# Kernel optimization log

Measured on AMD Instinct MI355X. Metric: run time of the kernel, lower is better.

## Reference

```python
import jax, jax.numpy as jnp
import numpy as np

B = 65536      # batch
N_IN = 784     # n_input_neurons
D = 10         # n_neurons_per_hidd_bank
NB = 10        # banks per layer (layer0 = input banks 0-9, layer1 = output banks 10-19)
N_OUT = 10     # n_output_neurons
N_HIDD_BANKS = 20


def setup_inputs() -> dict:
    key = jax.random.key(0)
    ks = jax.random.split(key, 10)
    s_in = 1.0 / np.sqrt(N_IN)
    s_d = 1.0 / np.sqrt(D)
    return {
        "x": jax.random.normal(ks[0], (B, N_IN), dtype=jnp.float32),
        # input-bank linears: 784 -> 10, one per input bank
        "W_in": jax.random.uniform(ks[1], (NB, N_IN, D), jnp.float32, -s_in, s_in),
        "b_in": jax.random.uniform(ks[2], (NB, D), jnp.float32, -s_in, s_in),
        # gate linears per (source, target) connection: 10 -> 1
        "W_gate": jax.random.uniform(ks[3], (NB, NB, D), jnp.float32, -s_d, s_d),
        "b_gate": jax.random.uniform(ks[4], (NB, NB), jnp.float32, -s_d, s_d),
        # data linears per (source, target) connection: 10 -> 10
        "W_data": jax.random.uniform(ks[5], (NB, NB, D, D), jnp.float32, -s_d, s_d),
        "b_data": jax.random.uniform(ks[6], (NB, NB, D), jnp.float32, -s_d, s_d),
        # output-bank linears: 10 -> 10, one per output bank
        "W_out": jax.random.uniform(ks[7], (NB, D, N_OUT), jnp.float32, -s_d, s_d),
        "b_out": jax.random.uniform(ks[8], (NB, N_OUT), jnp.float32, -s_d, s_d),
    }


def reference(x, W_in, b_in, W_gate, b_gate, W_data, b_data, W_out, b_out):
    # Input banks (banks 0-9): relu(Linear_784->10)
    acts0 = jax.nn.relu(jnp.einsum("bi,sid->sbd", x, W_in) + b_in[:, None, :])  # [S,B,D]

    # Gates: original checks gate_act.data[0,0] > 0, i.e. scalar from batch row 0 only.
    gate = jnp.einsum("sd,std->st", acts0[:, 0, :], W_gate) + b_gate  # [S,T]
    mask = (gate > 0.0).astype(x.dtype)                               # [S,T] binary, detached

    # Per-connection data linears (bias included per open connection, as in original)
    data = jnp.einsum("sbd,stde->stbe", acts0, W_data) + b_data[:, :, None, :]  # [S,T,B,D]
    target_pre = jnp.einsum("st,stbe->tbe", mask, data)                          # [T,B,D]
    acts1 = jax.nn.relu(target_pre)                                              # [T,B,D]

    # A target bank is active (non-None) iff any incoming gate is open; its output
    # linear (including bias) only contributes when active.
    any_open = (jnp.sum(mask, axis=0) > 0.0).astype(x.dtype)  # [T]
    out_contrib = jnp.einsum("tbe,teo->tbo", acts1, W_out) + b_out[:, None, :]
    logits = jnp.einsum("t,tbo->bo", any_open, out_contrib)   # [B,N_OUT]

    output = jax.nn.log_softmax(logits, axis=1)
    prob_open_gate = jnp.sum(mask) / N_HIDD_BANKS
    return output, prob_open_gate
```

## Files before the change

kernel.cpp:

```cpp
#include <hip/hip_runtime.h>
#include <math.h>

#define BATCH   65536
#define N_IN    784
#define DD      10
#define NB      10
#define SD      100
#define N_OUTS  10
#define TILES   16
#define ROWST   16

typedef float  f32x4  __attribute__((ext_vector_type(4)));
typedef short  bf16x8 __attribute__((ext_vector_type(8)));

#define WTF_F 0
#define WDF_F 51200
#define WOF_F 59392
#define BD_F  60416
#define WO_F  60544
#define BL_F  61664
#define MK_F  61680

__device__ __forceinline__ short f2bf(float f) {
    unsigned u = __builtin_bit_cast(unsigned, f);
    unsigned r = u + 0x7fffu + ((u >> 16) & 1u);
    return (short)(r >> 16);
}

__device__ __forceinline__ bf16x8 pack8cvt(f32x4 lo, f32x4 hi) {
    union { unsigned u[4]; bf16x8 v; } o;
    asm("v_cvt_pk_bf16_f32 %0, %1, %2" : "=v"(o.u[0]) : "v"(lo[0]), "v"(lo[1]));
    asm("v_cvt_pk_bf16_f32 %0, %1, %2" : "=v"(o.u[1]) : "v"(lo[2]), "v"(lo[3]));
    asm("v_cvt_pk_bf16_f32 %0, %1, %2" : "=v"(o.u[2]) : "v"(hi[0]), "v"(hi[1]));
    asm("v_cvt_pk_bf16_f32 %0, %1, %2" : "=v"(o.u[3]) : "v"(hi[2]), "v"(hi[3]));
    return o.v;
}

#define VMCNT0_BAR() do {                                        \
    asm volatile("s_waitcnt vmcnt(0)" ::: "memory");             \
    __builtin_amdgcn_s_barrier();                                \
    __builtin_amdgcn_sched_barrier(0); } while (0)

#define BAR_LGKM() do {                                          \
    asm volatile("s_waitcnt lgkmcnt(0)" ::: "memory");           \
    __builtin_amdgcn_s_barrier();                                \
    __builtin_amdgcn_sched_barrier(0); } while (0)

__global__ __launch_bounds__(1024) void prep1_kernel(
                             const float* __restrict__ x,
                             const float* __restrict__ W_in,
                             const float* __restrict__ b_in,
                             const float* __restrict__ W_gate,
                             const float* __restrict__ b_gate,
                             const float* __restrict__ b_data,
                             const float* __restrict__ W_out,
                             const float* __restrict__ b_out,
                             float* __restrict__ out,
                             float* __restrict__ ws) {
    __shared__ float a0r0[SD];
    __shared__ float mask_l[SD];
    __shared__ float ao_l[NB];
    const int tid = threadIdx.x;

    if (tid < 800) {
        int c = tid >> 3, h = tid & 7;
        int s = c / DD, d = c % DD;
        const float* wcol = W_in + s * (N_IN * DD) + d;
        float acc = 0.f;
        int i0 = h * 98;
        #pragma unroll 14
        for (int i = i0; i < i0 + 98; ++i)
            acc += x[i] * wcol[i * DD];
        acc += __shfl_xor(acc, 1, 64);
        acc += __shfl_xor(acc, 2, 64);
        acc += __shfl_xor(acc, 4, 64);
        if (h == 0) a0r0[c] = fmaxf(acc + b_in[c], 0.f);
    }
    __syncthreads();

    if (tid < SD) {
        float g = b_gate[tid];
        int s = tid / DD;
        for (int d = 0; d < DD; ++d)
            g += a0r0[s * DD + d] * W_gate[tid * DD + d];
        mask_l[tid] = (g > 0.f) ? 1.f : 0.f;
    }
    __syncthreads();

    if (tid < NB) {
        float any = 0.f;
        for (int s = 0; s < NB; ++s) any = fmaxf(any, mask_l[s * DD + tid]);
        ao_l[tid] = any;
    }
    if (tid == 0) {
        float sum = 0.f;
        for (int i = 0; i < SD; ++i) sum += mask_l[i];
        out[(long)BATCH * N_OUTS] = sum / 20.0f;
    }
    __syncthreads();

    if (tid < SD) ws[MK_F + tid] = mask_l[tid];

    for (int idx = tid; idx < 128; idx += blockDim.x) {
        float v = 0.f;
        if (idx < SD) {
            int t = idx / DD, e = idx % DD;
            for (int s = 0; s < NB; ++s)
                v += mask_l[s * DD + t] * b_data[(s * NB + t) * DD + e];
        }
        ws[BD_F + idx] = v;
    }
    for (int idx = tid; idx < 10 * 112; idx += blockDim.x) {
        int o = idx / 112, te = idx % 112;
        float v = 0.f;
        if (te < SD) {
            int t = te / DD, e = te % DD;
            v = ao_l[t] * W_out[(t * DD + e) * N_OUTS + o];
        }
        ws[WO_F + idx] = v;
    }
    if (tid < N_OUTS) {
        float v = 0.f;
        for (int t = 0; t < NB; ++t) v += ao_l[t] * b_out[t * N_OUTS + tid];
        ws[BL_F + tid] = v;
    }
}

__global__ void prep2_kernel(const float* __restrict__ W_in,
                             const float* __restrict__ W_data,
                             float* __restrict__ ws) {
    short* wtf = (short*)(ws + WTF_F);
    short* wdf = (short*)(ws + WDF_F);
    short* wof = (short*)(ws + WOF_F);
    const float* mask = ws + MK_F;
    const int n1 = 25 * 8 * 512;
    const int n2 = 4 * 8 * 512;
    const int n3 = 4 * 512;
    for (int idx = blockIdx.x * blockDim.x + threadIdx.x; idx < n1 + n2 + n3;
         idx += gridDim.x * blockDim.x) {
        if (idx < n1) {
            int K = idx / 4096, rem = idx % 4096;
            int ct = rem / 512, l2 = rem % 512;
            int l = l2 >> 3, e = l2 & 7;
            int r = l & 15, g = l >> 4;
            int c = 16 * ct + r, k = K * 32 + g * 8 + e;
            float v = (c < SD && k < N_IN)
                          ? W_in[(c / DD) * (N_IN * DD) + k * DD + (c % DD)] : 0.f;
            wtf[idx] = f2bf(v);
        } else if (idx < n1 + n2) {
            int i2 = idx - n1;
            int kk = i2 / 4096, rem = i2 % 4096;
            int ct = rem / 512, l2 = rem % 512;
            int l = l2 >> 3, e = l2 & 7;
            int r = l & 15, g = l >> 4;
            int m = 16 * ct + r, k = kk * 32 + g * 8 + e;
            float v = 0.f;
            if (m < SD && k < SD) {
                int t = m / DD, eo = m % DD, s = k / DD, d = k % DD;
                v = mask[s * DD + t] * W_data[((s * NB + t) * DD + d) * DD + eo];
            }
            wdf[i2] = f2bf(v);
        } else {
            int i3 = idx - n1 - n2;
            int kk = i3 / 512, l2 = i3 % 512;
            int l = l2 >> 3, e = l2 & 7;
            int o = l & 15, g = l >> 4;
            int te = kk * 32 + g * 8 + e;
            float v = (o < 10 && te < 112) ? ws[WO_F + o * 112 + te] : 0.f;
            wof[i3] = f2bf(v);
        }
    }
}

__global__ __launch_bounds__(512, 2) void main_kernel(
        const float* __restrict__ x,
        const float* __restrict__ b_in,
        const float* __restrict__ ws,
        float* __restrict__ out) {
    __shared__ __align__(16) unsigned char ldsx[2][50176];
    __shared__ __align__(16) short a0b[16 * 136];
    __shared__ __align__(16) short a1b[16 * 136];

    const int tid  = threadIdx.x;
    const int w    = tid >> 6;
    const int lane = tid & 63;
    const int g    = lane >> 4;
    const int r    = lane & 15;
    const size_t rowbase = (size_t)blockIdx.x * (TILES * ROWST);
    const char* xblk = (const char*)x + rowbase * (N_IN * 4);

    const short* wtf = (const short*)(ws + WTF_F);
    const short* wdf = (const short*)(ws + WDF_F);
    const short* wof = (const short*)(ws + WOF_F);

    bf16x8 wt[25];
    #pragma unroll
    for (int K = 0; K < 25; ++K)
        wt[K] = *(const bf16x8*)(wtf + (K * 8 + w) * 512 + lane * 8);
    bf16x8 wd[4], wo[4];
    #pragma unroll
    for (int kk = 0; kk < 4; ++kk) {
        wd[kk] = *(const bf16x8*)(wdf + (kk * 8 + w) * 512 + lane * 8);
        wo[kk] = *(const bf16x8*)(wof + kk * 512 + lane * 8);
    }
    float bi[4], bd[4], blv[4];
    #pragma unroll
    for (int j = 0; j < 4; ++j) {
        int c = 16 * w + 4 * g + j;
        bi[j] = (c < SD) ? b_in[c] : 0.f;
        bd[j] = ws[BD_F + c];
        int o = 4 * g + j;
        blv[j] = (o < 10) ? ws[BL_F + o] : 0.f;
    }

#define STAGE(t, buf) do {                                                     \
    const char* _src = xblk + (size_t)(t) * 50176;                             \
    _Pragma("unroll")                                                          \
    for (int _q = 0; _q < 7; ++_q) {                                           \
        int _I = w + 8 * _q;                                                   \
        if (_I < 49) {                                                         \
            __builtin_amdgcn_global_load_lds(                                  \
                (const __attribute__((address_space(1))) unsigned int*)        \
                    (_src + _I * 1024 + lane * 16),                            \
                (__attribute__((address_space(3))) unsigned int*)              \
                    (&ldsx[buf][0] + _I * 1024),                               \
                16, 0, 0);                                                     \
        }                                                                      \
    }                                                                          \
} while (0)

    STAGE(0, 0);

    for (int t = 0; t < TILES; ++t) {
        const int cur = t & 1;
        VMCNT0_BAR();
        if (t + 1 < TILES) STAGE(t + 1, cur ^ 1);

        f32x4 acc = (f32x4){0.f, 0.f, 0.f, 0.f};
        const unsigned char* xb = &ldsx[cur][0] + r * 3136 + g * 32;
        #pragma unroll
        for (int K = 0; K < 25; ++K) {
            const unsigned char* p = xb + K * 128;
            if (K == 24 && g >= 2) p = xb;
            f32x4 lo = *(const f32x4*)(p);
            f32x4 hi = *(const f32x4*)(p + 16);
            bf16x8 bf = pack8cvt(lo, hi);
            acc = __builtin_amdgcn_mfma_f32_16x16x32_bf16(wt[K], bf, acc, 0, 0, 0);
        }
        {
            short* myrow = a0b + r * 136;
            int c0 = 16 * w + 4 * g;
            float v0 = fmaxf(acc[0] + bi[0], 0.f), v1 = fmaxf(acc[1] + bi[1], 0.f);
            float v2 = fmaxf(acc[2] + bi[2], 0.f), v3 = fmaxf(acc[3] + bi[3], 0.f);
            unsigned p01, p23;
            asm("v_cvt_pk_bf16_f32 %0, %1, %2" : "=v"(p01) : "v"(v0), "v"(v1));
            asm("v_cvt_pk_bf16_f32 %0, %1, %2" : "=v"(p23) : "v"(v2), "v"(v3));
            *(uint2*)(myrow + c0) = make_uint2(p01, p23);
        }
        BAR_LGKM();

        f32x4 acc2 = (f32x4){0.f, 0.f, 0.f, 0.f};
        #pragma unroll
        for (int kk = 0; kk < 4; ++kk) {
            bf16x8 bf = *(const bf16x8*)(a0b + r * 136 + kk * 32 + g * 8);
            acc2 = __builtin_amdgcn_mfma_f32_16x16x32_bf16(wd[kk], bf, acc2, 0, 0, 0);
        }
        {
            short* myrow = a1b + r * 136;
            int c0 = 16 * w + 4 * g;
            float v0 = fmaxf(acc2[0] + bd[0], 0.f), v1 = fmaxf(acc2[1] + bd[1], 0.f);
            float v2 = fmaxf(acc2[2] + bd[2], 0.f), v3 = fmaxf(acc2[3] + bd[3], 0.f);
            unsigned p01, p23;
            asm("v_cvt_pk_bf16_f32 %0, %1, %2" : "=v"(p01) : "v"(v0), "v"(v1));
            asm("v_cvt_pk_bf16_f32 %0, %1, %2" : "=v"(p23) : "v"(v2), "v"(v3));
            *(uint2*)(myrow + c0) = make_uint2(p01, p23);
        }
        BAR_LGKM();

        f32x4 accL = (f32x4){0.f, 0.f, 0.f, 0.f};
        #pragma unroll
        for (int kk = 0; kk < 4; ++kk) {
            bf16x8 bf = *(const bf16x8*)(a1b + r * 136 + kk * 32 + g * 8);
            accL = __builtin_amdgcn_mfma_f32_16x16x32_bf16(wo[kk], bf, accL, 0, 0, 0);
        }
        float lgf[4];
        #pragma unroll
        for (int j = 0; j < 4; ++j)
            lgf[j] = (4 * g + j < 10) ? accL[j] + blv[j] : -1e30f;

        float m = fmaxf(fmaxf(lgf[0], lgf[1]), fmaxf(lgf[2], lgf[3]));
        m = fmaxf(m, __shfl_xor(m, 16, 64));
        m = fmaxf(m, __shfl_xor(m, 32, 64));
        float s = expf(lgf[0] - m) + expf(lgf[1] - m)
                + expf(lgf[2] - m) + expf(lgf[3] - m);
        s += __shfl_xor(s, 16, 64);
        s += __shfl_xor(s, 32, 64);
        float z = m + logf(s);

        if ((r >> 1) == w) {
            float* ob = out + (rowbase + (size_t)t * ROWST + r) * N_OUTS + 4 * g;
            if (g < 3) *(float2*)(ob)     = make_float2(lgf[0] - z, lgf[1] - z);
            if (g < 2) *(float2*)(ob + 2) = make_float2(lgf[2] - z, lgf[3] - z);
        }
    }
#undef STAGE
}

extern "C" void kernel_launch(void* const* d_in, const int* in_sizes, int n_in,
                              void* d_out, int out_size, void* d_ws, size_t ws_size,
                              hipStream_t stream) {
    const float* x      = (const float*)d_in[0];
    const float* W_in   = (const float*)d_in[1];
    const float* b_in   = (const float*)d_in[2];
    const float* W_gate = (const float*)d_in[3];
    const float* b_gate = (const float*)d_in[4];
    const float* W_data = (const float*)d_in[5];
    const float* b_data = (const float*)d_in[6];
    const float* W_out  = (const float*)d_in[7];
    const float* b_out  = (const float*)d_in[8];
    float* out = (float*)d_out;
    float* ws  = (float*)d_ws;

    prep1_kernel<<<1, 1024, 0, stream>>>(x, W_in, b_in, W_gate, b_gate,
                                         b_data, W_out, b_out, out, ws);
    prep2_kernel<<<256, 256, 0, stream>>>(W_in, W_data, ws);
    main_kernel<<<256, 512, 0, stream>>>(x, b_in, ws, out);
}
```

Baseline: 83.44 us.

## Convert staged x tile to bf16 once in shared memory before MFMA loop

Adds a cooperative pass that converts each staged fp32 x tile to a padded bf16 buffer in LDS, with zeroed tail padding, so the MFMA loop reads ready bf16 fragments. Previously each of 8 waves redundantly loaded fp32 and converted the same x data. This adds an extra barrier and LDS buffer per tile. The larger LDS footprint leads to lowering launch bounds to one block per CU, reducing occupancy.

```diff
diff --git a/kernel.cpp b/kernel.cpp
--- a/kernel.cpp
+++ b/kernel.cpp
@@ -9,6 +9,7 @@
 #define N_OUTS  10
 #define TILES   16
 #define ROWST   16
+#define XSTRIDE 1616
 
 typedef float  f32x4  __attribute__((ext_vector_type(4)));
 typedef short  bf16x8 __attribute__((ext_vector_type(8)));
@@ -25,15 +26,6 @@
     unsigned u = __builtin_bit_cast(unsigned, f);
     unsigned r = u + 0x7fffu + ((u >> 16) & 1u);
     return (short)(r >> 16);
-}
-
-__device__ __forceinline__ bf16x8 pack8cvt(f32x4 lo, f32x4 hi) {
-    union { unsigned u[4]; bf16x8 v; } o;
-    asm("v_cvt_pk_bf16_f32 %0, %1, %2" : "=v"(o.u[0]) : "v"(lo[0]), "v"(lo[1]));
-    asm("v_cvt_pk_bf16_f32 %0, %1, %2" : "=v"(o.u[1]) : "v"(lo[2]), "v"(lo[3]));
-    asm("v_cvt_pk_bf16_f32 %0, %1, %2" : "=v"(o.u[2]) : "v"(hi[0]), "v"(hi[1]));
-    asm("v_cvt_pk_bf16_f32 %0, %1, %2" : "=v"(o.u[3]) : "v"(hi[2]), "v"(hi[3]));
-    return o.v;
 }
 
 #define VMCNT0_BAR() do {                                        \
@@ -172,12 +164,13 @@
     }
 }
 
-__global__ __launch_bounds__(512, 2) void main_kernel(
+__global__ __launch_bounds__(512, 1) void main_kernel(
         const float* __restrict__ x,
         const float* __restrict__ b_in,
         const float* __restrict__ ws,
         float* __restrict__ out) {
     __shared__ __align__(16) unsigned char ldsx[2][50176];
+    __shared__ __align__(16) unsigned char xb16[16 * XSTRIDE];
     __shared__ __align__(16) short a0b[16 * 136];
     __shared__ __align__(16) short a1b[16 * 136];
 
@@ -236,15 +229,28 @@
         VMCNT0_BAR();
         if (t + 1 < TILES) STAGE(t + 1, cur ^ 1);
 
+        {
+            const f32x4* src = (const f32x4*)&ldsx[cur][0];
+            for (int q = tid; q < 3136; q += 512) {
+                int row = q / 196, col4 = q - row * 196;
+                f32x4 v = src[q];
+                unsigned p01, p23;
+                asm("v_cvt_pk_bf16_f32 %0, %1, %2" : "=v"(p01) : "v"(v[0]), "v"(v[1]));
+                asm("v_cvt_pk_bf16_f32 %0, %1, %2" : "=v"(p23) : "v"(v[2]), "v"(v[3]));
+                *(uint2*)(xb16 + row * XSTRIDE + col4 * 8) = make_uint2(p01, p23);
+            }
+            if (tid < 96) {
+                int row = tid / 6, part = tid - row * 6;
+                *(uint2*)(xb16 + row * XSTRIDE + 1568 + part * 8) = make_uint2(0u, 0u);
+            }
+        }
+        BAR_LGKM();
+
         f32x4 acc = (f32x4){0.f, 0.f, 0.f, 0.f};
-        const unsigned char* xb = &ldsx[cur][0] + r * 3136 + g * 32;
+        const unsigned char* xb = xb16 + r * XSTRIDE + g * 16;
         #pragma unroll
         for (int K = 0; K < 25; ++K) {
-            const unsigned char* p = xb + K * 128;
-            if (K == 24 && g >= 2) p = xb;
-            f32x4 lo = *(const f32x4*)(p);
-            f32x4 hi = *(const f32x4*)(p + 16);
-            bf16x8 bf = pack8cvt(lo, hi);
+            bf16x8 bf = *(const bf16x8*)(xb + K * 64);
             acc = __builtin_amdgcn_mfma_f32_16x16x32_bf16(wt[K], bf, acc, 0, 0, 0);
         }
         {
```

Measured after the change: 84.53 us. About the same (+1.3%).
